# Kernel tuning notes

Hardware: AMD Instinct MI355X
Metric: run time of the kernel (lower is better)

Reference implementation:

```python
import jax, jax.numpy as jnp
import numpy as np

KH, KW = 3, 3
STRIDE = 1
PADDING = 1
CIN, COUT = 64, 64


def setup_inputs() -> dict:
    key = jax.random.key(0)
    kx, kw, kb = jax.random.split(key, 3)
    x = jax.random.normal(kx, (16, CIN, 112, 112), dtype=jnp.float32)
    # Kaiming-uniform style init, matching the torch module
    fan = CIN * KH * KW
    gain = np.sqrt(2.0)
    bound_w = np.sqrt(3.0) * gain / np.sqrt(fan)
    weights = jax.random.uniform(kw, (COUT, CIN, KH, KW), dtype=jnp.float32,
                                 minval=-bound_w, maxval=bound_w)
    bound_b = 1.0 / np.sqrt(fan)
    bias = jax.random.uniform(kb, (COUT,), dtype=jnp.float32,
                              minval=-bound_b, maxval=bound_b)
    return {"x": x, "weights": weights, "bias": bias}


def reference(x, weights, bias):
    # Equivalent to F.unfold + GEMM: a standard cross-correlation conv.
    # x: (N, C, H, W), weights: (F, C, KH, KW) -> out: (N, F, H', W')
    out = jax.lax.conv_general_dilated(
        x, weights,
        window_strides=(STRIDE, STRIDE),
        padding=((PADDING, PADDING), (PADDING, PADDING)),
        dimension_numbers=("NCHW", "OIHW", "NCHW"),
    )
    return out + bias[None, :, None, None]
```

## Files before the change

### kernel.cpp

```cpp
#include <hip/hip_runtime.h>


typedef __attribute__((ext_vector_type(8))) short bf16x8;
typedef __attribute__((ext_vector_type(4))) float f32x4;

#define CIN 64
#define COUT 64
#define HH 112
#define WW 112
#define ROWS 2
#define DYS  4

#define XP 72
#define WCOLS 114
#define LDS_SHORTS (DYS * WCOLS * XP)

__device__ __forceinline__ unsigned short f2bf(float f) {
    unsigned u = __builtin_bit_cast(unsigned, f);
    u += 0x7FFFu + ((u >> 16) & 1u);
    return (unsigned short)(u >> 16);
}

#if __has_builtin(__builtin_amdgcn_cvt_pk_bf16_f32)
__device__ __forceinline__ unsigned pk2bf(float a, float b) {
    typedef __attribute__((ext_vector_type(2))) __bf16 bf16x2;
    bf16x2 r = __builtin_amdgcn_cvt_pk_bf16_f32(a, b);
    return __builtin_bit_cast(unsigned, r);
}
#else
__device__ __forceinline__ unsigned pk2bf(float a, float b) {
    return (unsigned)f2bf(a) | ((unsigned)f2bf(b) << 16);
}
#endif

__global__ void conv_wprep(const float* __restrict__ w, short* __restrict__ wbf) {
    int i = blockIdx.x * 256 + threadIdx.x;
    int j = i & 7;
    int f = (i >> 3) & 63;
    int koct = (i >> 9) & 3;
    int cb = (i >> 11) & 1;
    int t = i >> 12;
    int c = cb * 32 + koct * 8 + j;
    int ky = t / 3, kx = t - ky * 3;
    wbf[i] = (short)f2bf(w[((f * CIN + c) * 3 + ky) * 3 + kx]);
}

__global__ __launch_bounds__(256, 2)
void conv3x3_mfma(const float* __restrict__ x, const short* __restrict__ wbf,
                  const float* __restrict__ bias, float* __restrict__ out)
{
    __shared__ __align__(16) short lds[LDS_SHORTS];
    const int tid = threadIdx.x;
    const int n = blockIdx.x;
    const int h0 = blockIdx.y * ROWS;

    const int wave = tid >> 6;
    const int r  = wave >> 1;
    const int nh = wave & 1;
    const int lane = tid & 63;
    const int lm = lane & 15;
    const int q  = lane >> 4;

    if (tid < 128) {
        int e = tid & 15;
        int g = tid >> 4;
        int dy = g >> 1;
        int wcol = (g & 1) ? (WCOLS - 1) : 0;
        *(uint2*)&lds[((dy * WCOLS + wcol) * 36 + e * 2) * 2] = (uint2){0u, 0u};
    }
    if (h0 == 0) {
        for (int i = tid; i < WCOLS * 16; i += 256) {
            int wcol = i >> 4, e = i & 15;
            *(uint2*)&lds[((0 * WCOLS + wcol) * 36 + e * 2) * 2] = (uint2){0u, 0u};
        }
    }
    if (h0 == HH - ROWS) {
        for (int i = tid; i < WCOLS * 16; i += 256) {
            int wcol = i >> 4, e = i & 15;
            *(uint2*)&lds[(((DYS - 1) * WCOLS + wcol) * 36 + e * 2) * 2] = (uint2){0u, 0u};
        }
    }
    for (int i = tid; i < DYS * 16 * 28; i += 256) {
        int w4 = i % 28;
        int rp = i / 28;
        int dy = rp >> 4;
        int cq = rp & 15;
        int gh = h0 + dy - 1;
        if ((unsigned)gh < (unsigned)HH) {
            int c = cq * 4;
            const float* px = x + (((n * CIN + c) * HH + gh) * WW + w4 * 4);
            const float4 v0 = *(const float4*)px;
            const float4 v1 = *(const float4*)(px + HH * WW);
            const float4 v2 = *(const float4*)(px + 2 * HH * WW);
            const float4 v3 = *(const float4*)(px + 3 * HH * WW);
            int o = cq >> 1, p = cq & 1;
            float a0[4] = {v0.x, v0.y, v0.z, v0.w};
            float a1[4] = {v1.x, v1.y, v1.z, v1.w};
            float a2[4] = {v2.x, v2.y, v2.z, v2.w};
            float a3[4] = {v3.x, v3.y, v3.z, v3.w};
#pragma unroll
            for (int dw = 0; dw < 4; ++dw) {
                int wcol = 1 + w4 * 4 + dw;
                int swz = (wcol >> 2) & 7;
                int dslot = 4 * (o ^ swz) + 2 * p;
                uint2 pk;
                pk.x = pk2bf(a0[dw], a1[dw]);
                pk.y = pk2bf(a2[dw], a3[dw]);
                *(uint2*)&lds[((dy * WCOLS + wcol) * 36 + dslot) * 2] = pk;
            }
        }
    }

    bf16x8 br[2][2][2];
#pragma unroll
    for (int ntl = 0; ntl < 2; ++ntl) {
        int f = (nh * 2 + ntl) * 16 + lm;
        br[0][ntl][0] = *(const bf16x8*)(wbf + (q) * 512 + f * 8);
        br[0][ntl][1] = *(const bf16x8*)(wbf + (4 + q) * 512 + f * 8);
    }

    __syncthreads();

    f32x4 acc[7][2];
#pragma unroll
    for (int mt = 0; mt < 7; ++mt)
#pragma unroll
        for (int ntl = 0; ntl < 2; ++ntl) acc[mt][ntl] = (f32x4){0.f, 0.f, 0.f, 0.f};

#pragma unroll
    for (int t = 0; t < 9; ++t) {
        const int buf = t & 1;
        if (t < 8) {
#pragma unroll
            for (int ntl = 0; ntl < 2; ++ntl) {
                int f = (nh * 2 + ntl) * 16 + lm;
                br[1 - buf][ntl][0] = *(const bf16x8*)(wbf + ((t + 1) * 8 + q) * 512 + f * 8);
                br[1 - buf][ntl][1] = *(const bf16x8*)(wbf + ((t + 1) * 8 + 4 + q) * 512 + f * 8);
            }
        }
        const int ky = t / 3, kx = t - ky * 3;
#pragma unroll
        for (int mt = 0; mt < 7; ++mt) {
            int wcol = mt * 16 + lm + kx;
            int swz = (wcol >> 2) & 7;
            int base = ((r + ky) * WCOLS + wcol) * XP;
            bf16x8 a0 = *(const bf16x8*)&lds[base + 8 * (q ^ swz)];
            bf16x8 a1 = *(const bf16x8*)&lds[base + 8 * ((q + 4) ^ swz)];
#pragma unroll
            for (int ntl = 0; ntl < 2; ++ntl)
                acc[mt][ntl] = __builtin_amdgcn_mfma_f32_16x16x32_bf16(a0, br[buf][ntl][0], acc[mt][ntl], 0, 0, 0);
#pragma unroll
            for (int ntl = 0; ntl < 2; ++ntl)
                acc[mt][ntl] = __builtin_amdgcn_mfma_f32_16x16x32_bf16(a1, br[buf][ntl][1], acc[mt][ntl], 0, 0, 0);
        }
    }

    __syncthreads();
    float* lout = (float*)lds;
#pragma unroll
    for (int mt = 0; mt < 7; ++mt)
#pragma unroll
        for (int ntl = 0; ntl < 2; ++ntl) {
            const f32x4 v = acc[mt][ntl];
            int fr = r * 64 + (nh * 2 + ntl) * 16 + lm;
#pragma unroll
            for (int rr = 0; rr < 4; ++rr)
                lout[fr * 113 + mt * 16 + q * 4 + rr] = v[rr];
        }
    __syncthreads();
    for (int i = tid; i < 128 * 28; i += 256) {
        int fr = i / 28;
        int w4 = i - fr * 28;
        int rw = fr >> 6;
        int f = fr & 63;
        float b = bias[f];
        const float* lp = lout + fr * 113 + w4 * 4;
        float4 v;
        v.x = lp[0] + b; v.y = lp[1] + b; v.z = lp[2] + b; v.w = lp[3] + b;
        *(float4*)(out + (((n * COUT + f) * HH + h0 + rw) * WW + w4 * 4)) = v;
    }
}

extern "C" void kernel_launch(void* const* d_in, const int* in_sizes, int n_in,
                              void* d_out, int out_size, void* d_ws, size_t ws_size,
                              hipStream_t stream) {
    const float* x = (const float*)d_in[0];
    const float* w = (const float*)d_in[1];
    const float* b = (const float*)d_in[2];
    float* out = (float*)d_out;
    short* wbf = (short*)d_ws;

    conv_wprep<<<144, 256, 0, stream>>>(w, wbf);
    dim3 grid(16, HH / ROWS);
    conv3x3_mfma<<<grid, 256, 0, stream>>>(x, wbf, b, out);
}
```

Baseline: 121.5 us.

## Split width into two halves per block with octet-planar LDS and direct stores

Adds a grid z dimension that splits each row pair's 112 columns into a 64-wide and a 48-wide half. Each block now holds a smaller octet-planar LDS tile with halo columns loaded separately, and launch bounds rise to 4 blocks per CU. The epilogue writes MFMA accumulators plus bias straight to global memory instead of staging them through LDS, which removes two barriers. The aim is more parallelism and occupancy from smaller blocks with fewer accumulators. The cost is halo re-reads, uneven work between the two halves, an unswizzled LDS layout that may cause bank conflicts, and narrower global stores.

```diff
diff --git a/kernel.cpp b/kernel.cpp
--- a/kernel.cpp
+++ b/kernel.cpp
@@ -10,10 +10,13 @@
 #define WW 112
 #define ROWS 2
 #define DYS  4
-
-#define XP 72
-#define WCOLS 114
-#define LDS_SHORTS (DYS * WCOLS * XP)
+#define WCMAX 66
+#define PLANE (8 * WCMAX * 8)
+#define LDS_SHORTS (DYS * PLANE)
+
+__device__ __forceinline__ int ladr(int dy, int oct, int w) {
+    return ((dy * 8 + oct) * WCMAX + w) * 8;
+}
 
 __device__ __forceinline__ unsigned short f2bf(float f) {
     unsigned u = __builtin_bit_cast(unsigned, f);
@@ -45,7 +48,39 @@
     wbf[i] = (short)f2bf(w[((f * CIN + c) * 3 + ky) * 3 + kx]);
 }
 
-__global__ __launch_bounds__(256, 2)
+template<int MT>
+__device__ __forceinline__ void main_loop(const short* lds, const short* __restrict__ wbf,
+                                          f32x4 (&acc)[4][2], bf16x8 (&br)[2][2][2],
+                                          int r, int nh, int lm, int q)
+{
+#pragma unroll
+    for (int t = 0; t < 9; ++t) {
+        const int buf = t & 1;
+        if (t < 8) {
+#pragma unroll
+            for (int ntl = 0; ntl < 2; ++ntl) {
+                const int f = (nh * 2 + ntl) * 16 + lm;
+                br[1 - buf][ntl][0] = *(const bf16x8*)(wbf + ((t + 1) * 8 + q) * 512 + f * 8);
+                br[1 - buf][ntl][1] = *(const bf16x8*)(wbf + ((t + 1) * 8 + 4 + q) * 512 + f * 8);
+            }
+        }
+        const int ky = t / 3, kx = t - ky * 3;
+#pragma unroll
+        for (int mt = 0; mt < MT; ++mt) {
+            const int wcol = mt * 16 + lm + kx;
+            const bf16x8 a0 = *(const bf16x8*)&lds[ladr(r + ky, q, wcol)];
+            const bf16x8 a1 = *(const bf16x8*)&lds[ladr(r + ky, q + 4, wcol)];
+#pragma unroll
+            for (int ntl = 0; ntl < 2; ++ntl)
+                acc[mt][ntl] = __builtin_amdgcn_mfma_f32_16x16x32_bf16(a0, br[buf][ntl][0], acc[mt][ntl], 0, 0, 0);
+#pragma unroll
+            for (int ntl = 0; ntl < 2; ++ntl)
+                acc[mt][ntl] = __builtin_amdgcn_mfma_f32_16x16x32_bf16(a1, br[buf][ntl][1], acc[mt][ntl], 0, 0, 0);
+        }
+    }
+}
+
+__global__ __launch_bounds__(256, 4)
 void conv3x3_mfma(const float* __restrict__ x, const short* __restrict__ wbf,
                   const float* __restrict__ bias, float* __restrict__ out)
 {
@@ -53,6 +88,9 @@
     const int tid = threadIdx.x;
     const int n = blockIdx.x;
     const int h0 = blockIdx.y * ROWS;
+    const int ws = blockIdx.z;
+    const int MTN = ws ? 3 : 4;
+    const int c0 = ws * 64;
 
     const int wave = tid >> 6;
     const int r  = wave >> 1;
@@ -61,123 +99,91 @@
     const int lm = lane & 15;
     const int q  = lane >> 4;
 
-    if (tid < 128) {
-        int e = tid & 15;
-        int g = tid >> 4;
-        int dy = g >> 1;
-        int wcol = (g & 1) ? (WCOLS - 1) : 0;
-        *(uint2*)&lds[((dy * WCOLS + wcol) * 36 + e * 2) * 2] = (uint2){0u, 0u};
+    if (tid < 32) {
+        const int dy = tid >> 3, oct = tid & 7;
+        const int padw = ws ? 49 : 0;
+        *(uint4*)&lds[ladr(dy, oct, padw)] = (uint4){0u, 0u, 0u, 0u};
     }
     if (h0 == 0) {
-        for (int i = tid; i < WCOLS * 16; i += 256) {
-            int wcol = i >> 4, e = i & 15;
-            *(uint2*)&lds[((0 * WCOLS + wcol) * 36 + e * 2) * 2] = (uint2){0u, 0u};
-        }
+        uint4* p = (uint4*)&lds[0];
+        for (int i = tid; i < PLANE / 8; i += 256) p[i] = (uint4){0u, 0u, 0u, 0u};
     }
     if (h0 == HH - ROWS) {
-        for (int i = tid; i < WCOLS * 16; i += 256) {
-            int wcol = i >> 4, e = i & 15;
-            *(uint2*)&lds[(((DYS - 1) * WCOLS + wcol) * 36 + e * 2) * 2] = (uint2){0u, 0u};
-        }
-    }
-    for (int i = tid; i < DYS * 16 * 28; i += 256) {
-        int w4 = i % 28;
-        int rp = i / 28;
-        int dy = rp >> 4;
-        int cq = rp & 15;
-        int gh = h0 + dy - 1;
+        uint4* p = (uint4*)&lds[(DYS - 1) * PLANE];
+        for (int i = tid; i < PLANE / 8; i += 256) p[i] = (uint4){0u, 0u, 0u, 0u};
+    }
+    {
+        const int W4N = ws ? 12 : 16;
+        const int dy = tid >> 6, oct = (tid >> 3) & 7, w4lo = tid & 7;
+        const int gh = h0 + dy - 1;
         if ((unsigned)gh < (unsigned)HH) {
-            int c = cq * 4;
-            const float* px = x + (((n * CIN + c) * HH + gh) * WW + w4 * 4);
-            const float4 v0 = *(const float4*)px;
-            const float4 v1 = *(const float4*)(px + HH * WW);
-            const float4 v2 = *(const float4*)(px + 2 * HH * WW);
-            const float4 v3 = *(const float4*)(px + 3 * HH * WW);
-            int o = cq >> 1, p = cq & 1;
-            float a0[4] = {v0.x, v0.y, v0.z, v0.w};
-            float a1[4] = {v1.x, v1.y, v1.z, v1.w};
-            float a2[4] = {v2.x, v2.y, v2.z, v2.w};
-            float a3[4] = {v3.x, v3.y, v3.z, v3.w};
-#pragma unroll
-            for (int dw = 0; dw < 4; ++dw) {
-                int wcol = 1 + w4 * 4 + dw;
-                int swz = (wcol >> 2) & 7;
-                int dslot = 4 * (o ^ swz) + 2 * p;
-                uint2 pk;
-                pk.x = pk2bf(a0[dw], a1[dw]);
-                pk.y = pk2bf(a2[dw], a3[dw]);
-                *(uint2*)&lds[((dy * WCOLS + wcol) * 36 + dslot) * 2] = pk;
+            for (int w4 = w4lo; w4 < W4N; w4 += 8) {
+                const float* px = x + (((n * CIN + oct * 8) * HH + gh) * WW + c0 + w4 * 4);
+                float v[8][4];
+#pragma unroll
+                for (int k = 0; k < 8; ++k) {
+                    const float4 t = *(const float4*)(px + k * HH * WW);
+                    v[k][0] = t.x; v[k][1] = t.y; v[k][2] = t.z; v[k][3] = t.w;
+                }
+#pragma unroll
+                for (int dw = 0; dw < 4; ++dw) {
+                    uint4 pk;
+                    pk.x = pk2bf(v[0][dw], v[1][dw]);
+                    pk.y = pk2bf(v[2][dw], v[3][dw]);
+                    pk.z = pk2bf(v[4][dw], v[5][dw]);
+                    pk.w = pk2bf(v[6][dw], v[7][dw]);
+                    *(uint4*)&lds[ladr(dy, oct, 1 + w4 * 4 + dw)] = pk;
+                }
             }
         }
     }
+    {
+        const int dy = tid >> 6, c = tid & 63;
+        const int gh = h0 + dy - 1;
+        const int gce = ws ? 63 : 64;
+        const int wedge = ws ? 0 : 65;
+        if ((unsigned)gh < (unsigned)HH) {
+            const float vv = x[((n * CIN + c) * HH + gh) * WW + gce];
+            lds[ladr(dy, c >> 3, wedge) + (c & 7)] = (short)f2bf(vv);
+        }
+    }
 
     bf16x8 br[2][2][2];
 #pragma unroll
     for (int ntl = 0; ntl < 2; ++ntl) {
-        int f = (nh * 2 + ntl) * 16 + lm;
+        const int f = (nh * 2 + ntl) * 16 + lm;
         br[0][ntl][0] = *(const bf16x8*)(wbf + (q) * 512 + f * 8);
         br[0][ntl][1] = *(const bf16x8*)(wbf + (4 + q) * 512 + f * 8);
     }
 
     __syncthreads();
 
-    f32x4 acc[7][2];
-#pragma unroll
-    for (int mt = 0; mt < 7; ++mt)
+    f32x4 acc[4][2];
+#pragma unroll
+    for (int mt = 0; mt < 4; ++mt)
 #pragma unroll
         for (int ntl = 0; ntl < 2; ++ntl) acc[mt][ntl] = (f32x4){0.f, 0.f, 0.f, 0.f};
 
-#pragma unroll
-    for (int t = 0; t < 9; ++t) {
-        const int buf = t & 1;
-        if (t < 8) {
+    if (MTN == 4) main_loop<4>(lds, wbf, acc, br, r, nh, lm, q);
+    else          main_loop<3>(lds, wbf, acc, br, r, nh, lm, q);
+
+    const int f0 = nh * 32 + lm;
+    const float b0 = bias[f0];
+    const float b1 = bias[f0 + 16];
+    const int hrow = h0 + r;
+#pragma unroll
+    for (int mt = 0; mt < 4; ++mt) {
+        if (mt < MTN) {
 #pragma unroll
             for (int ntl = 0; ntl < 2; ++ntl) {
-                int f = (nh * 2 + ntl) * 16 + lm;
-                br[1 - buf][ntl][0] = *(const bf16x8*)(wbf + ((t + 1) * 8 + q) * 512 + f * 8);
-                br[1 - buf][ntl][1] = *(const bf16x8*)(wbf + ((t + 1) * 8 + 4 + q) * 512 + f * 8);
+                const f32x4 v = acc[mt][ntl];
+                const float bb = ntl ? b1 : b0;
+                float4 s;
+                s.x = v[0] + bb; s.y = v[1] + bb; s.z = v[2] + bb; s.w = v[3] + bb;
+                const int f = f0 + ntl * 16;
+                *(float4*)(out + ((n * COUT + f) * HH + hrow) * WW + c0 + mt * 16 + q * 4) = s;
             }
         }
-        const int ky = t / 3, kx = t - ky * 3;
-#pragma unroll
-        for (int mt = 0; mt < 7; ++mt) {
-            int wcol = mt * 16 + lm + kx;
-            int swz = (wcol >> 2) & 7;
-            int base = ((r + ky) * WCOLS + wcol) * XP;
-            bf16x8 a0 = *(const bf16x8*)&lds[base + 8 * (q ^ swz)];
-            bf16x8 a1 = *(const bf16x8*)&lds[base + 8 * ((q + 4) ^ swz)];
-#pragma unroll
-            for (int ntl = 0; ntl < 2; ++ntl)
-                acc[mt][ntl] = __builtin_amdgcn_mfma_f32_16x16x32_bf16(a0, br[buf][ntl][0], acc[mt][ntl], 0, 0, 0);
-#pragma unroll
-            for (int ntl = 0; ntl < 2; ++ntl)
-                acc[mt][ntl] = __builtin_amdgcn_mfma_f32_16x16x32_bf16(a1, br[buf][ntl][1], acc[mt][ntl], 0, 0, 0);
-        }
-    }
-
-    __syncthreads();
-    float* lout = (float*)lds;
-#pragma unroll
-    for (int mt = 0; mt < 7; ++mt)
-#pragma unroll
-        for (int ntl = 0; ntl < 2; ++ntl) {
-            const f32x4 v = acc[mt][ntl];
-            int fr = r * 64 + (nh * 2 + ntl) * 16 + lm;
-#pragma unroll
-            for (int rr = 0; rr < 4; ++rr)
-                lout[fr * 113 + mt * 16 + q * 4 + rr] = v[rr];
-        }
-    __syncthreads();
-    for (int i = tid; i < 128 * 28; i += 256) {
-        int fr = i / 28;
-        int w4 = i - fr * 28;
-        int rw = fr >> 6;
-        int f = fr & 63;
-        float b = bias[f];
-        const float* lp = lout + fr * 113 + w4 * 4;
-        float4 v;
-        v.x = lp[0] + b; v.y = lp[1] + b; v.z = lp[2] + b; v.w = lp[3] + b;
-        *(float4*)(out + (((n * COUT + f) * HH + h0 + rw) * WW + w4 * 4)) = v;
     }
 }
 
@@ -191,6 +197,6 @@
     short* wbf = (short*)d_ws;
 
     conv_wprep<<<144, 256, 0, stream>>>(w, wbf);
-    dim3 grid(16, HH / ROWS);
+    dim3 grid(16, HH / ROWS, 2);
     conv3x3_mfma<<<grid, 256, 0, stream>>>(x, wbf, b, out);
 }
```

Result: slower. 125.1 us (+2.9%).
